# Kernel optimization log

Hardware: AMD Instinct MI355X
Metric: run time of the kernel (lower is better)

## Reference

```python
import jax, jax.numpy as jnp
import numpy as np

# e2m1 FP4 value table: sign bit in nibble MSB, values {0,0.5,1,1.5,2,3,4,6}
_E2M1 = jnp.array([0.0, 0.5, 1.0, 1.5, 2.0, 3.0, 4.0, 6.0,
                   -0.0, -0.5, -1.0, -1.5, -2.0, -3.0, -4.0, -6.0], dtype=jnp.float32)


def _dequant_fp4(packed, scales, group_size):
    """packed: [E, out, in//8] uint32; scales: [E, in//group_size, out] -> [E, out, in] f32."""
    shifts = jnp.arange(8, dtype=jnp.uint32) * 4  # nibble shift amounts 0,4,...,28
    nib = (packed[..., None] >> shifts) & jnp.uint32(0xF)  # [E, out, in//8, 8]
    E, O, P, _ = nib.shape
    nib = nib.reshape(E, O, P * 8).astype(jnp.int32)
    w = _E2M1[nib]  # [E, out, in] f32
    gids = jnp.arange(P * 8) // group_size  # group id per input column
    sc = jnp.transpose(scales, (0, 2, 1))[:, :, gids]  # [E, out, in]
    return w * sc


def setup_inputs() -> dict:
    E, H, I, T, K, G = 8, 2048, 1408, 2048, 2, 128
    key = jax.random.key(0)
    ks = jax.random.split(key, 9)
    x = jax.random.normal(ks[0], (T, H), dtype=jnp.float32)
    gate_packed = jax.random.bits(ks[1], (E, I, H // 8), dtype=jnp.uint32)
    up_packed = jax.random.bits(ks[2], (E, I, H // 8), dtype=jnp.uint32)
    down_packed = jax.random.bits(ks[3], (E, H, I // 8), dtype=jnp.uint32)
    gate_scales = jax.random.uniform(ks[4], (E, H // G, I), jnp.float32, 0.5, 1.5)
    up_scales = jax.random.uniform(ks[5], (E, H // G, I), jnp.float32, 0.5, 1.5)
    down_scales = jax.random.uniform(ks[6], (E, I // G, H), jnp.float32, 0.5, 1.5)
    topk_idx = jax.random.randint(ks[7], (T, K), 0, E, dtype=jnp.int32)
    w = jax.random.uniform(ks[8], (T, K), jnp.float32)
    topk_w = w / jnp.sum(w, axis=-1, keepdims=True)
    return {"x": x,
            "gate_packed": gate_packed, "gate_scales": gate_scales,
            "up_packed": up_packed, "up_scales": up_scales,
            "down_packed": down_packed, "down_scales": down_scales,
            "topk_idx": topk_idx, "topk_w": topk_w, "group_size": G}


def reference(x, gate_packed, gate_scales, up_packed, up_scales,
              down_packed, down_scales, topk_idx, topk_w, group_size):
    # Fused dequant (nibble unpack + e2m1 table + per-group scale) for all experts
    gate_w = _dequant_fp4(gate_packed, gate_scales, group_size)  # [E, I, H]
    up_w = _dequant_fp4(up_packed, up_scales, group_size)        # [E, I, H]
    down_w = _dequant_fp4(down_packed, down_scales, group_size)  # [E, H, I]
    # Grouped SwiGLU expert MLP (dense over E=8 experts, gather routed outputs)
    g = jnp.einsum('th,eih->eti', x, gate_w)
    u = jnp.einsum('th,eih->eti', x, up_w)
    h = jax.nn.silu(g) * u                                        # [E, T, I]
    y = jnp.einsum('eti,ehi->eth', h, down_w)                     # [E, T, H]
    T = x.shape[0]
    sel = y[topk_idx, jnp.arange(T)[:, None], :]                  # [T, K, H]
    return jnp.sum(sel * topk_w[..., None], axis=1)               # [T, H]
```

## Files before the change

kernel.cpp:

```cpp
#include <hip/hip_runtime.h>
#include <hip/hip_bf16.h>
#include <stdint.h>

#define E_ 8
#define H_ 2048
#define I_ 1408
#define T_ 2048
#define K_ 2
#define G_ 128

typedef __bf16 bf16;
typedef bf16 bf16x8 __attribute__((ext_vector_type(8)));
typedef float f32x4 __attribute__((ext_vector_type(4)));

__device__ __forceinline__ uint32_t prm(uint32_t hi, uint32_t lo, uint32_t sel) {
    return __builtin_amdgcn_perm(hi, lo, sel);
}

struct DequantTab { uint32_t thi0, thi1, tlo0, tlo1; };

__device__ __forceinline__ DequantTab build_tab(float s) {
    union { bf16 h[8]; uint32_t u[4]; } tb;
    tb.h[0] = (bf16)(0.0f);
    tb.h[1] = (bf16)(0.5f * s);
    tb.h[2] = (bf16)(1.0f * s);
    tb.h[3] = (bf16)(1.5f * s);
    tb.h[4] = (bf16)(2.0f * s);
    tb.h[5] = (bf16)(3.0f * s);
    tb.h[6] = (bf16)(4.0f * s);
    tb.h[7] = (bf16)(6.0f * s);
    DequantTab t;
    t.thi0 = prm(tb.u[1], tb.u[0], 0x07050301u);
    t.tlo0 = prm(tb.u[1], tb.u[0], 0x06040200u);
    t.thi1 = prm(tb.u[3], tb.u[2], 0x07050301u);
    t.tlo1 = prm(tb.u[3], tb.u[2], 0x06040200u);
    return t;
}

__device__ __forceinline__ uint4 dequant8t(uint32_t p, const DequantTab& t) {
    const uint32_t pr = p >> 4;
    const uint32_t pe = p  & 0x07070707u;
    const uint32_t po = pr & 0x07070707u;
    const uint32_t He = prm(t.thi1, t.thi0, pe) | ((p  & 0x08080808u) << 4);
    const uint32_t Le = prm(t.tlo1, t.tlo0, pe);
    const uint32_t Ho = prm(t.thi1, t.thi0, po) | ((pr & 0x08080808u) << 4);
    const uint32_t Lo = prm(t.tlo1, t.tlo0, po);
    const uint32_t E01 = prm(He, Le, 0x05010400u);
    const uint32_t E23 = prm(He, Le, 0x07030602u);
    const uint32_t O01 = prm(Ho, Lo, 0x05010400u);
    const uint32_t O23 = prm(Ho, Lo, 0x07030602u);
    return make_uint4(prm(O01, E01, 0x05040100u),
                      prm(O01, E01, 0x07060302u),
                      prm(O23, E23, 0x05040100u),
                      prm(O23, E23, 0x07060302u));
}

__device__ __forceinline__ void gld16(void* lds, const void* g) {
    __builtin_amdgcn_global_load_lds(
        (__attribute__((address_space(1))) void*)g,
        (__attribute__((address_space(3))) void*)lds, 16, 0, 0);
}

#define SB0() __builtin_amdgcn_sched_barrier(0)

#define DQW(WD, PW, TAB) do { \
    uint4 d0_ = dequant8t((PW).x, (TAB)); \
    uint4 d1_ = dequant8t((PW).y, (TAB)); \
    uint4 d2_ = dequant8t((PW).z, (TAB)); \
    uint4 d3_ = dequant8t((PW).w, (TAB)); \
    *(uint4*)&WD[wrow][((cb + 0) ^ rs) * 8] = d0_; \
    *(uint4*)&WD[wrow][((cb + 1) ^ rs) * 8] = d1_; \
    *(uint4*)&WD[wrow][((cb + 2) ^ rs) * 8] = d2_; \
    *(uint4*)&WD[wrow][((cb + 3) ^ rs) * 8] = d3_; \
} while (0)

__global__ void route_count(const int* __restrict__ topk_idx, int* __restrict__ counts) {
    int p = blockIdx.x * blockDim.x + threadIdx.x;
    if (p < T_ * K_) atomicAdd(&counts[topk_idx[p]], 1);
}

__global__ void route_scan(const int* __restrict__ counts, int* __restrict__ offsets,
                           int* __restrict__ tmap) {
    if (threadIdx.x == 0) {
        int acc = 0, ti = 0;
        for (int e = 0; e < E_; e++) {
            offsets[e] = acc;
            int nt = (counts[e] + 127) >> 7;
            for (int j = 0; j < nt; j++) tmap[ti++] = (e << 16) | j;
            acc += counts[e];
        }
        offsets[E_] = acc;
        offsets[E_ + 1] = ti;
        for (; ti < 64; ti++) tmap[ti] = -1;
    }
}

__global__ void route_fill(const int* __restrict__ topk_idx, const float* __restrict__ topk_w,
                           int* __restrict__ cursors, const int* __restrict__ offsets,
                           int* __restrict__ tok, float* __restrict__ wgt,
                           int* __restrict__ inv) {
    int p = blockIdx.x * blockDim.x + threadIdx.x;
    if (p < T_ * K_) {
        int e = topk_idx[p];
        int slot = atomicAdd(&cursors[e], 1);
        int idx = offsets[e] + slot;
        tok[idx] = p / K_;
        wgt[idx] = topk_w[p];
        inv[p] = idx;
    }
}

__global__ __launch_bounds__(256)
void xcast_kernel(const float* __restrict__ x, uint4* __restrict__ xb) {
    const int i = blockIdx.x * 256 + threadIdx.x;
    const float4 a = ((const float4*)x)[i * 2];
    const float4 b = ((const float4*)x)[i * 2 + 1];
    union { uint4 u; bf16 h[8]; } r;
    r.h[0] = (bf16)a.x; r.h[1] = (bf16)a.y; r.h[2] = (bf16)a.z; r.h[3] = (bf16)a.w;
    r.h[4] = (bf16)b.x; r.h[5] = (bf16)b.y; r.h[6] = (bf16)b.z; r.h[7] = (bf16)b.w;
    xb[i] = r.u;
}

__global__ __launch_bounds__(256, 2)
void gemm1t_kernel(const bf16* __restrict__ xb,
                   const uint32_t* __restrict__ gate_packed,
                   const float* __restrict__ gate_scales,
                   const uint32_t* __restrict__ up_packed,
                   const float* __restrict__ up_scales,
                   const int* __restrict__ offsets,
                   const int* __restrict__ tmap,
                   const int* __restrict__ tok, bf16* __restrict__ h_buf)
{
    __shared__ __align__(16) bf16 xs0[128][64];
    __shared__ __align__(16) bf16 xs1[128][64];
    __shared__ __align__(16) bf16 wgs0[64][64];
    __shared__ __align__(16) bf16 wgs1[64][64];
    __shared__ __align__(16) bf16 wus0[64][64];
    __shared__ __align__(16) bf16 wus1[64][64];

    const int tid = threadIdx.x;
    const int ntiles = offsets[E_ + 1];
    const int nwork = ntiles * 22;

    const int xr = tid >> 3;
    const int xc = tid & 7;
    const int xch = (xc ^ (xr & 7)) * 8;

    const int mat  = tid >> 7;
    const int id   = tid & 127;
    const int wrow = id >> 1;
    const int quad = id & 1;
    const int cb = quad * 4, rs = wrow & 7;

    const int wave = tid >> 6, lane = tid & 63;
    const int wy = wave >> 1, wx = wave & 1;
    const int lrow = lane & 15, kq = lane >> 4;

    constexpr int NG = H_ / G_;

#define MFMA1(XS, WG, WU) do { \
    _Pragma("unroll") \
    for (int kh = 0; kh < 2; ++kh) { \
        bf16x8 a[4], bg[2], bu[2]; \
        _Pragma("unroll") \
        for (int mi = 0; mi < 4; ++mi) { \
            const int ra = wy * 64 + mi * 16 + lrow; \
            a[mi] = *(const bf16x8*)&XS[ra][((kh * 4 + kq) ^ (ra & 7)) * 8]; \
        } \
        _Pragma("unroll") \
        for (int ni = 0; ni < 2; ++ni) { \
            const int rbq = wx * 32 + ni * 16 + lrow; \
            const int cbq = ((kh * 4 + kq) ^ (rbq & 7)) * 8; \
            bg[ni] = *(const bf16x8*)&WG[rbq][cbq]; \
            bu[ni] = *(const bf16x8*)&WU[rbq][cbq]; \
        } \
        _Pragma("unroll") \
        for (int mi = 0; mi < 4; ++mi) \
            _Pragma("unroll") \
            for (int ni = 0; ni < 2; ++ni) { \
                accg[mi][ni] = __builtin_amdgcn_mfma_f32_16x16x32_bf16(a[mi], bg[ni], accg[mi][ni], 0, 0, 0); \
                accu[mi][ni] = __builtin_amdgcn_mfma_f32_16x16x32_bf16(a[mi], bu[ni], accu[mi][ni], 0, 0, 0); \
            } \
    } \
} while (0)

    for (int wk = blockIdx.x; wk < nwork; wk += gridDim.x) {
        const int wt = wk / 22;
        const int itile = wk - wt * 22;
        const int tm = tmap[wt];
        const int e = tm >> 16, ty = tm & 0xffff;
        const int row0 = offsets[e];
        const int cnt = offsets[e + 1] - row0;

        const bf16* xsrc[4];
        bf16 *xdst0[4], *xdst1[4];
#pragma unroll
        for (int j = 0; j < 4; ++j) {
            int g = ty * 128 + xr + j * 32;
            g = (g < cnt) ? g : (cnt - 1);
            xsrc[j] = xb + (size_t)tok[row0 + g] * H_ + xch;
            xdst0[j] = &xs0[xr + j * 32][xc * 8];
            xdst1[j] = &xs1[xr + j * 32][xc * 8];
        }

        const int irow = itile * 64 + wrow;
        const uint32_t* wp_row = (mat ? up_packed : gate_packed)
            + (size_t)e * I_ * (H_ / 8) + (size_t)irow * (H_ / 8) + quad * 4;
        const float* ws_row = (mat ? up_scales : gate_scales)
            + (size_t)e * (H_ / G_) * I_ + irow;
        bf16 (* const wd0)[64] = mat ? wus0 : wgs0;
        bf16 (* const wd1)[64] = mat ? wus1 : wgs1;

        f32x4 accg[4][2] = {};
        f32x4 accu[4][2] = {};

#pragma unroll
        for (int j = 0; j < 4; ++j) gld16(xdst0[j], xsrc[j]);
        SB0();
        uint4 pw0 = *(const uint4*)(wp_row);
        uint4 pwO = *(const uint4*)(wp_row + 8);
        float sc0 = ws_row[0];
        SB0();
        DequantTab tab = build_tab(sc0);
        DQW(wd0, pw0, tab);
        asm volatile("s_waitcnt lgkmcnt(0)" ::: "memory");
        __builtin_amdgcn_s_barrier();
        SB0();

        float scn = 0.f;
        uint4 pwE;
        for (int kg = 0; kg < NG; ++kg) {
            const bool last = (kg == NG - 1);
#pragma unroll
            for (int j = 0; j < 4; ++j) gld16(xdst1[j], xsrc[j] + (kg * 2 + 1) * 64);
            SB0();
            if (!last) {
                pwE = *(const uint4*)(wp_row + (size_t)(kg * 2 + 2) * 8);
                scn = ws_row[(size_t)(kg + 1) * I_];
            }
            SB0();
            DQW(wd1, pwO, tab);
            MFMA1(xs0, wgs0, wus0);
            SB0();
            if (!last) asm volatile("s_waitcnt vmcnt(2) lgkmcnt(0)" ::: "memory");
            else       asm volatile("s_waitcnt vmcnt(0) lgkmcnt(0)" ::: "memory");
            __builtin_amdgcn_s_barrier();
            SB0();

            if (!last) {
#pragma unroll
                for (int j = 0; j < 4; ++j) gld16(xdst0[j], xsrc[j] + (kg * 2 + 2) * 64);
                SB0();
                pwO = *(const uint4*)(wp_row + (size_t)(kg * 2 + 3) * 8);
                SB0();
                tab = build_tab(scn);
                DQW(wd0, pwE, tab);
                MFMA1(xs1, wgs1, wus1);
                SB0();
                asm volatile("s_waitcnt vmcnt(1) lgkmcnt(0)" ::: "memory");
                __builtin_amdgcn_s_barrier();
                SB0();
            } else {
                MFMA1(xs1, wgs1, wus1);
                SB0();
                asm volatile("s_waitcnt lgkmcnt(0)" ::: "memory");
                __builtin_amdgcn_s_barrier();
                SB0();
            }
        }

#pragma unroll
        for (int mi = 0; mi < 4; ++mi)
#pragma unroll
            for (int ni = 0; ni < 2; ++ni) {
                const int icol = itile * 64 + wx * 32 + ni * 16 + lrow;
#pragma unroll
                for (int r = 0; r < 4; ++r) {
                    const int grow = ty * 128 + wy * 64 + mi * 16 + kq * 4 + r;
                    if (grow < cnt) {
                        const float gv = accg[mi][ni][r];
                        const float hv = gv / (1.f + __expf(-gv)) * accu[mi][ni][r];
                        h_buf[(size_t)(row0 + grow) * I_ + icol] = (bf16)hv;
                    }
                }
            }
        __builtin_amdgcn_s_barrier();
    }
#undef MFMA1
}

__global__ __launch_bounds__(256, 2)
void gemm2t_kernel(const bf16* __restrict__ h_buf,
                   const uint32_t* __restrict__ down_packed,
                   const float* __restrict__ down_scales,
                   const int* __restrict__ offsets,
                   const int* __restrict__ tmap,
                   const float* __restrict__ wgt, float* __restrict__ yp)
{
    __shared__ __align__(16) bf16 hs0[128][64];
    __shared__ __align__(16) bf16 hs1[128][64];
    __shared__ __align__(16) bf16 wds0[128][64];
    __shared__ __align__(16) bf16 wds1[128][64];

    const int tid = threadIdx.x;
    const int ntiles = offsets[E_ + 1];
    const int nwork = ntiles * 16;

    const int xr = tid >> 3;
    const int xc = tid & 7;
    const int xch = (xc ^ (xr & 7)) * 8;

    const int wrow = tid >> 1;
    const int quad = tid & 1;
    const int cb = quad * 4, rs = wrow & 7;

    const int wave = tid >> 6, lane = tid & 63;
    const int wy = wave >> 1, wx = wave & 1;
    const int lrow = lane & 15, kq = lane >> 4;

    constexpr int NG = I_ / G_;

#define MFMA2(HS, WD) do { \
    _Pragma("unroll") \
    for (int kh = 0; kh < 2; ++kh) { \
        bf16x8 a[4], b[4]; \
        _Pragma("unroll") \
        for (int mi = 0; mi < 4; ++mi) { \
            const int ra = wy * 64 + mi * 16 + lrow; \
            a[mi] = *(const bf16x8*)&HS[ra][((kh * 4 + kq) ^ (ra & 7)) * 8]; \
        } \
        _Pragma("unroll") \
        for (int ni = 0; ni < 4; ++ni) { \
            const int rbq = wx * 64 + ni * 16 + lrow; \
            b[ni] = *(const bf16x8*)&WD[rbq][((kh * 4 + kq) ^ (rbq & 7)) * 8]; \
        } \
        _Pragma("unroll") \
        for (int mi = 0; mi < 4; ++mi) \
            _Pragma("unroll") \
            for (int ni = 0; ni < 4; ++ni) \
                acc[mi][ni] = __builtin_amdgcn_mfma_f32_16x16x32_bf16(a[mi], b[ni], acc[mi][ni], 0, 0, 0); \
    } \
} while (0)

    for (int wk = blockIdx.x; wk < nwork; wk += gridDim.x) {
        const int wt = wk >> 4;
        const int htile = wk & 15;
        const int tm = tmap[wt];
        const int e = tm >> 16, ty = tm & 0xffff;
        const int row0 = offsets[e];
        const int cnt = offsets[e + 1] - row0;

        const bf16* hsrc[4];
        bf16 *hdst0[4], *hdst1[4];
#pragma unroll
        for (int j = 0; j < 4; ++j) {
            int g = ty * 128 + xr + j * 32;
            g = (g < cnt) ? g : (cnt - 1);
            hsrc[j] = h_buf + (size_t)(row0 + g) * I_ + xch;
            hdst0[j] = &hs0[xr + j * 32][xc * 8];
            hdst1[j] = &hs1[xr + j * 32][xc * 8];
        }

        const int hrow = htile * 128 + wrow;
        const uint32_t* dp_row = down_packed + (size_t)e * H_ * (I_ / 8) + (size_t)hrow * (I_ / 8) + quad * 4;
        const float* ds_row = down_scales + (size_t)e * (I_ / G_) * H_ + hrow;

        f32x4 acc[4][4] = {};

#pragma unroll
        for (int j = 0; j < 4; ++j) gld16(hdst0[j], hsrc[j]);
        SB0();
        uint4 pw0 = *(const uint4*)(dp_row);
        uint4 pwO = *(const uint4*)(dp_row + 8);
        float sc0 = ds_row[0];
        SB0();
        DequantTab tab = build_tab(sc0);
        DQW(wds0, pw0, tab);
        asm volatile("s_waitcnt lgkmcnt(0)" ::: "memory");
        __builtin_amdgcn_s_barrier();
        SB0();

        float scn = 0.f;
        uint4 pwE;
        for (int kg = 0; kg < NG; ++kg) {
            const bool last = (kg == NG - 1);
#pragma unroll
            for (int j = 0; j < 4; ++j) gld16(hdst1[j], hsrc[j] + (kg * 2 + 1) * 64);
            SB0();
            if (!last) {
                pwE = *(const uint4*)(dp_row + (size_t)(kg * 2 + 2) * 8);
                scn = ds_row[(size_t)(kg + 1) * H_];
            }
            SB0();
            DQW(wds1, pwO, tab);
            MFMA2(hs0, wds0);
            SB0();
            if (!last) asm volatile("s_waitcnt vmcnt(2) lgkmcnt(0)" ::: "memory");
            else       asm volatile("s_waitcnt vmcnt(0) lgkmcnt(0)" ::: "memory");
            __builtin_amdgcn_s_barrier();
            SB0();

            if (!last) {
#pragma unroll
                for (int j = 0; j < 4; ++j) gld16(hdst0[j], hsrc[j] + (kg * 2 + 2) * 64);
                SB0();
                pwO = *(const uint4*)(dp_row + (size_t)(kg * 2 + 3) * 8);
                SB0();
                tab = build_tab(scn);
                DQW(wds0, pwE, tab);
                MFMA2(hs1, wds1);
                SB0();
                asm volatile("s_waitcnt vmcnt(1) lgkmcnt(0)" ::: "memory");
                __builtin_amdgcn_s_barrier();
                SB0();
            } else {
                MFMA2(hs1, wds1);
                SB0();
                asm volatile("s_waitcnt lgkmcnt(0)" ::: "memory");
                __builtin_amdgcn_s_barrier();
                SB0();
            }
        }

#pragma unroll
        for (int mi = 0; mi < 4; ++mi)
#pragma unroll
            for (int r = 0; r < 4; ++r) {
                const int lr = wy * 64 + mi * 16 + kq * 4 + r;
                const int grow = ty * 128 + lr;
                if (grow < cnt) {
                    const float w = wgt[row0 + grow];
#pragma unroll
                    for (int ni = 0; ni < 4; ++ni) {
                        const int col = htile * 128 + wx * 64 + ni * 16 + lrow;
                        yp[(size_t)(row0 + grow) * H_ + col] = acc[mi][ni][r] * w;
                    }
                }
            }
        __builtin_amdgcn_s_barrier();
    }
#undef MFMA2
}

__global__ __launch_bounds__(256)
void combine_kernel(const float* __restrict__ yp, const int* __restrict__ inv,
                    float* __restrict__ out) {
    const int idx = blockIdx.x * 256 + threadIdx.x;
    const int t = idx >> 9;
    const int c = idx & 511;
    const float4 a = ((const float4*)yp)[(size_t)inv[t * 2] * (H_ / 4) + c];
    const float4 b = ((const float4*)yp)[(size_t)inv[t * 2 + 1] * (H_ / 4) + c];
    float4 o;
    o.x = a.x + b.x; o.y = a.y + b.y; o.z = a.z + b.z; o.w = a.w + b.w;
    ((float4*)out)[idx] = o;
}

extern "C" void kernel_launch(void* const* d_in, const int* in_sizes, int n_in,
                              void* d_out, int out_size, void* d_ws, size_t ws_size,
                              hipStream_t stream) {
    const float* x = (const float*)d_in[0];
    const uint32_t* gate_packed = (const uint32_t*)d_in[1];
    const float* gate_scales = (const float*)d_in[2];
    const uint32_t* up_packed = (const uint32_t*)d_in[3];
    const float* up_scales = (const float*)d_in[4];
    const uint32_t* down_packed = (const uint32_t*)d_in[5];
    const float* down_scales = (const float*)d_in[6];
    const int* topk_idx = (const int*)d_in[7];
    const float* topk_w = (const float*)d_in[8];
    float* out = (float*)d_out;

    char* ws = (char*)d_ws;
    int* counts  = (int*)ws;
    int* cursors = (int*)(ws + 32);
    int* offsets = (int*)(ws + 64);
    int* tmap    = (int*)(ws + 128);
    int* tok     = (int*)(ws + 640);
    float* wgt   = (float*)(ws + 17024);
    int* inv     = (int*)(ws + 33408);
    bf16* h_buf  = (bf16*)(ws + 49792);
    bf16* xb     = (bf16*)(ws + 49792 + 11534336ull);
    float* yp    = (float*)(ws + 49792 + 11534336ull + 8388608ull);

    hipMemsetAsync(d_ws, 0, 1024, stream);

    route_count<<<(T_ * K_ + 255) / 256, 256, 0, stream>>>(topk_idx, counts);
    route_scan<<<1, 64, 0, stream>>>(counts, offsets, tmap);
    route_fill<<<(T_ * K_ + 255) / 256, 256, 0, stream>>>(topk_idx, topk_w, cursors, offsets,
                                                          tok, wgt, inv);
    xcast_kernel<<<T_ * H_ / 8 / 256, 256, 0, stream>>>(x, (uint4*)xb);

    gemm1t_kernel<<<512, 256, 0, stream>>>(xb, gate_packed, gate_scales, up_packed, up_scales,
                                           offsets, tmap, tok, h_buf);
    gemm2t_kernel<<<512, 256, 0, stream>>>(h_buf, down_packed, down_scales,
                                           offsets, tmap, wgt, yp);
    combine_kernel<<<T_ * H_ / 4 / 256, 256, 0, stream>>>(yp, inv, out);
}
```

Before: 273.3 us.

## Fuse top-k combine into down GEMM via atomics; single-buffer weight tiles for occupancy

Result: slower. 286.1 us (+4.7%).

```diff
diff --git a/kernel.cpp b/kernel.cpp
--- a/kernel.cpp
+++ b/kernel.cpp
@@ -97,8 +97,7 @@
 
 __global__ void route_fill(const int* __restrict__ topk_idx, const float* __restrict__ topk_w,
                            int* __restrict__ cursors, const int* __restrict__ offsets,
-                           int* __restrict__ tok, float* __restrict__ wgt,
-                           int* __restrict__ inv) {
+                           int* __restrict__ tok, float* __restrict__ wgt) {
     int p = blockIdx.x * blockDim.x + threadIdx.x;
     if (p < T_ * K_) {
         int e = topk_idx[p];
@@ -106,7 +105,6 @@
         int idx = offsets[e] + slot;
         tok[idx] = p / K_;
         wgt[idx] = topk_w[p];
-        inv[p] = idx;
     }
 }
 
@@ -121,7 +119,7 @@
     xb[i] = r.u;
 }
 
-__global__ __launch_bounds__(256, 2)
+__global__ __launch_bounds__(256, 3)
 void gemm1t_kernel(const bf16* __restrict__ xb,
                    const uint32_t* __restrict__ gate_packed,
                    const float* __restrict__ gate_scales,
@@ -133,10 +131,8 @@
 {
     __shared__ __align__(16) bf16 xs0[128][64];
     __shared__ __align__(16) bf16 xs1[128][64];
-    __shared__ __align__(16) bf16 wgs0[64][64];
-    __shared__ __align__(16) bf16 wgs1[64][64];
-    __shared__ __align__(16) bf16 wus0[64][64];
-    __shared__ __align__(16) bf16 wus1[64][64];
+    __shared__ __align__(16) bf16 wgs[64][64];
+    __shared__ __align__(16) bf16 wus[64][64];
 
     const int tid = threadIdx.x;
     const int ntiles = offsets[E_ + 1];
@@ -157,8 +153,9 @@
     const int lrow = lane & 15, kq = lane >> 4;
 
     constexpr int NG = H_ / G_;
-
-#define MFMA1(XS, WG, WU) do { \
+    constexpr int NT = 2 * NG;
+
+#define MFMA1(XS) do { \
     _Pragma("unroll") \
     for (int kh = 0; kh < 2; ++kh) { \
         bf16x8 a[4], bg[2], bu[2]; \
@@ -171,8 +168,8 @@
         for (int ni = 0; ni < 2; ++ni) { \
             const int rbq = wx * 32 + ni * 16 + lrow; \
             const int cbq = ((kh * 4 + kq) ^ (rbq & 7)) * 8; \
-            bg[ni] = *(const bf16x8*)&WG[rbq][cbq]; \
-            bu[ni] = *(const bf16x8*)&WU[rbq][cbq]; \
+            bg[ni] = *(const bf16x8*)&wgs[rbq][cbq]; \
+            bu[ni] = *(const bf16x8*)&wus[rbq][cbq]; \
         } \
         _Pragma("unroll") \
         for (int mi = 0; mi < 4; ++mi) \
@@ -208,8 +205,7 @@
             + (size_t)e * I_ * (H_ / 8) + (size_t)irow * (H_ / 8) + quad * 4;
         const float* ws_row = (mat ? up_scales : gate_scales)
             + (size_t)e * (H_ / G_) * I_ + irow;
-        bf16 (* const wd0)[64] = mat ? wus0 : wgs0;
-        bf16 (* const wd1)[64] = mat ? wus1 : wgs1;
+        bf16 (* const wd)[64] = mat ? wus : wgs;
 
         f32x4 accg[4][2] = {};
         f32x4 accu[4][2] = {};
@@ -217,56 +213,44 @@
 #pragma unroll
         for (int j = 0; j < 4; ++j) gld16(xdst0[j], xsrc[j]);
         SB0();
-        uint4 pw0 = *(const uint4*)(wp_row);
-        uint4 pwO = *(const uint4*)(wp_row + 8);
-        float sc0 = ws_row[0];
+        uint4 pw = *(const uint4*)(wp_row);
+        float sc = ws_row[0];
         SB0();
-        DequantTab tab = build_tab(sc0);
-        DQW(wd0, pw0, tab);
-        asm volatile("s_waitcnt lgkmcnt(0)" ::: "memory");
-        __builtin_amdgcn_s_barrier();
-        SB0();
-
-        float scn = 0.f;
-        uint4 pwE;
+
+        float scn = sc;
+        uint4 pwn;
         for (int kg = 0; kg < NG; ++kg) {
-            const bool last = (kg == NG - 1);
-#pragma unroll
-            for (int j = 0; j < 4; ++j) gld16(xdst1[j], xsrc[j] + (kg * 2 + 1) * 64);
-            SB0();
-            if (!last) {
-                pwE = *(const uint4*)(wp_row + (size_t)(kg * 2 + 2) * 8);
-                scn = ws_row[(size_t)(kg + 1) * I_];
-            }
-            SB0();
-            DQW(wd1, pwO, tab);
-            MFMA1(xs0, wgs0, wus0);
-            SB0();
-            if (!last) asm volatile("s_waitcnt vmcnt(2) lgkmcnt(0)" ::: "memory");
-            else       asm volatile("s_waitcnt vmcnt(0) lgkmcnt(0)" ::: "memory");
-            __builtin_amdgcn_s_barrier();
-            SB0();
-
-            if (!last) {
-#pragma unroll
-                for (int j = 0; j < 4; ++j) gld16(xdst0[j], xsrc[j] + (kg * 2 + 2) * 64);
-                SB0();
-                pwO = *(const uint4*)(wp_row + (size_t)(kg * 2 + 3) * 8);
-                SB0();
-                tab = build_tab(scn);
-                DQW(wd0, pwE, tab);
-                MFMA1(xs1, wgs1, wus1);
-                SB0();
-                asm volatile("s_waitcnt vmcnt(1) lgkmcnt(0)" ::: "memory");
+            const DequantTab tab = build_tab(sc);
+#pragma unroll
+            for (int kh2 = 0; kh2 < 2; ++kh2) {
+                const int t = kg * 2 + kh2;
+                const bool lastT = (t == NT - 1);
+                if (!lastT) {
+                    bf16* const* xd = kh2 ? xdst0 : xdst1;
+#pragma unroll
+                    for (int j = 0; j < 4; ++j) gld16(xd[j], xsrc[j] + (t + 1) * 64);
+                    SB0();
+                    pwn = *(const uint4*)(wp_row + (size_t)(t + 1) * 8);
+                    if (kh2 == 0) {
+                        const int kgn = (kg + 1 < NG) ? kg + 1 : kg;
+                        scn = ws_row[(size_t)kgn * I_];
+                    }
+                    SB0();
+                }
+                DQW(wd, pw, tab);
+                SB0();
+                if (!lastT) asm volatile("s_waitcnt vmcnt(6) lgkmcnt(0)" ::: "memory");
+                else        asm volatile("s_waitcnt vmcnt(0) lgkmcnt(0)" ::: "memory");
                 __builtin_amdgcn_s_barrier();
                 SB0();
-            } else {
-                MFMA1(xs1, wgs1, wus1);
+                if (kh2 == 0) MFMA1(xs0); else MFMA1(xs1);
                 SB0();
                 asm volatile("s_waitcnt lgkmcnt(0)" ::: "memory");
                 __builtin_amdgcn_s_barrier();
                 SB0();
+                pw = pwn;
             }
+            sc = scn;
         }
 
 #pragma unroll
@@ -284,23 +268,22 @@
                     }
                 }
             }
-        __builtin_amdgcn_s_barrier();
     }
 #undef MFMA1
 }
 
-__global__ __launch_bounds__(256, 2)
+__global__ __launch_bounds__(256, 3)
 void gemm2t_kernel(const bf16* __restrict__ h_buf,
                    const uint32_t* __restrict__ down_packed,
                    const float* __restrict__ down_scales,
                    const int* __restrict__ offsets,
                    const int* __restrict__ tmap,
-                   const float* __restrict__ wgt, float* __restrict__ yp)
+                   const int* __restrict__ tok,
+                   const float* __restrict__ wgt, float* __restrict__ out)
 {
     __shared__ __align__(16) bf16 hs0[128][64];
     __shared__ __align__(16) bf16 hs1[128][64];
-    __shared__ __align__(16) bf16 wds0[128][64];
-    __shared__ __align__(16) bf16 wds1[128][64];
+    __shared__ __align__(16) bf16 wds[128][64];
 
     const int tid = threadIdx.x;
     const int ntiles = offsets[E_ + 1];
@@ -319,8 +302,9 @@
     const int lrow = lane & 15, kq = lane >> 4;
 
     constexpr int NG = I_ / G_;
-
-#define MFMA2(HS, WD) do { \
+    constexpr int NT = 2 * NG;
+
+#define MFMA2(HS) do { \
     _Pragma("unroll") \
     for (int kh = 0; kh < 2; ++kh) { \
         bf16x8 a[4], b[4]; \
@@ -332,7 +316,7 @@
         _Pragma("unroll") \
         for (int ni = 0; ni < 4; ++ni) { \
             const int rbq = wx * 64 + ni * 16 + lrow; \
-            b[ni] = *(const bf16x8*)&WD[rbq][((kh * 4 + kq) ^ (rbq & 7)) * 8]; \
+            b[ni] = *(const bf16x8*)&wds[rbq][((kh * 4 + kq) ^ (rbq & 7)) * 8]; \
         } \
         _Pragma("unroll") \
         for (int mi = 0; mi < 4; ++mi) \
@@ -370,89 +354,64 @@
 #pragma unroll
         for (int j = 0; j < 4; ++j) gld16(hdst0[j], hsrc[j]);
         SB0();
-        uint4 pw0 = *(const uint4*)(dp_row);
-        uint4 pwO = *(const uint4*)(dp_row + 8);
-        float sc0 = ds_row[0];
+        uint4 pw = *(const uint4*)(dp_row);
+        float sc = ds_row[0];
         SB0();
-        DequantTab tab = build_tab(sc0);
-        DQW(wds0, pw0, tab);
-        asm volatile("s_waitcnt lgkmcnt(0)" ::: "memory");
-        __builtin_amdgcn_s_barrier();
-        SB0();
-
-        float scn = 0.f;
-        uint4 pwE;
+
+        float scn = sc;
+        uint4 pwn;
         for (int kg = 0; kg < NG; ++kg) {
-            const bool last = (kg == NG - 1);
-#pragma unroll
-            for (int j = 0; j < 4; ++j) gld16(hdst1[j], hsrc[j] + (kg * 2 + 1) * 64);
-            SB0();
-            if (!last) {
-                pwE = *(const uint4*)(dp_row + (size_t)(kg * 2 + 2) * 8);
-                scn = ds_row[(size_t)(kg + 1) * H_];
-            }
-            SB0();
-            DQW(wds1, pwO, tab);
-            MFMA2(hs0, wds0);
-            SB0();
-            if (!last) asm volatile("s_waitcnt vmcnt(2) lgkmcnt(0)" ::: "memory");
-            else       asm volatile("s_waitcnt vmcnt(0) lgkmcnt(0)" ::: "memory");
-            __builtin_amdgcn_s_barrier();
-            SB0();
-
-            if (!last) {
-#pragma unroll
-                for (int j = 0; j < 4; ++j) gld16(hdst0[j], hsrc[j] + (kg * 2 + 2) * 64);
-                SB0();
-                pwO = *(const uint4*)(dp_row + (size_t)(kg * 2 + 3) * 8);
-                SB0();
-                tab = build_tab(scn);
-                DQW(wds0, pwE, tab);
-                MFMA2(hs1, wds1);
-                SB0();
-                asm volatile("s_waitcnt vmcnt(1) lgkmcnt(0)" ::: "memory");
+            const DequantTab tab = build_tab(sc);
+#pragma unroll
+            for (int kh2 = 0; kh2 < 2; ++kh2) {
+                const int t = kg * 2 + kh2;
+                const bool lastT = (t == NT - 1);
+                if (!lastT) {
+                    bf16* const* hd = kh2 ? hdst0 : hdst1;
+#pragma unroll
+                    for (int j = 0; j < 4; ++j) gld16(hd[j], hsrc[j] + (t + 1) * 64);
+                    SB0();
+                    pwn = *(const uint4*)(dp_row + (size_t)(t + 1) * 8);
+                    if (kh2 == 0) {
+                        const int kgn = (kg + 1 < NG) ? kg + 1 : kg;
+                        scn = ds_row[(size_t)kgn * H_];
+                    }
+                    SB0();
+                }
+                DQW(wds, pw, tab);
+                SB0();
+                if (!lastT) asm volatile("s_waitcnt vmcnt(6) lgkmcnt(0)" ::: "memory");
+                else        asm volatile("s_waitcnt vmcnt(0) lgkmcnt(0)" ::: "memory");
                 __builtin_amdgcn_s_barrier();
                 SB0();
-            } else {
-                MFMA2(hs1, wds1);
+                if (kh2 == 0) MFMA2(hs0); else MFMA2(hs1);
                 SB0();
                 asm volatile("s_waitcnt lgkmcnt(0)" ::: "memory");
                 __builtin_amdgcn_s_barrier();
                 SB0();
+                pw = pwn;
             }
+            sc = scn;
         }
 
 #pragma unroll
         for (int mi = 0; mi < 4; ++mi)
 #pragma unroll
             for (int r = 0; r < 4; ++r) {
-                const int lr = wy * 64 + mi * 16 + kq * 4 + r;
-                const int grow = ty * 128 + lr;
+                const int grow = ty * 128 + wy * 64 + mi * 16 + kq * 4 + r;
                 if (grow < cnt) {
-                    const float w = wgt[row0 + grow];
+                    const int slot = row0 + grow;
+                    const float w = wgt[slot];
+                    const int tk = tok[slot];
 #pragma unroll
                     for (int ni = 0; ni < 4; ++ni) {
                         const int col = htile * 128 + wx * 64 + ni * 16 + lrow;
-                        yp[(size_t)(row0 + grow) * H_ + col] = acc[mi][ni][r] * w;
+                        atomicAdd(out + (size_t)tk * H_ + col, acc[mi][ni][r] * w);
                     }
                 }
             }
-        __builtin_amdgcn_s_barrier();
     }
 #undef MFMA2
-}
-
-__global__ __launch_bounds__(256)
-void combine_kernel(const float* __restrict__ yp, const int* __restrict__ inv,
-                    float* __restrict__ out) {
-    const int idx = blockIdx.x * 256 + threadIdx.x;
-    const int t = idx >> 9;
-    const int c = idx & 511;
-    const float4 a = ((const float4*)yp)[(size_t)inv[t * 2] * (H_ / 4) + c];
-    const float4 b = ((const float4*)yp)[(size_t)inv[t * 2 + 1] * (H_ / 4) + c];
-    float4 o;
-    o.x = a.x + b.x; o.y = a.y + b.y; o.z = a.z + b.z; o.w = a.w + b.w;
-    ((float4*)out)[idx] = o;
 }
 
 extern "C" void kernel_launch(void* const* d_in, const int* in_sizes, int n_in,
@@ -476,22 +435,20 @@
     int* tmap    = (int*)(ws + 128);
     int* tok     = (int*)(ws + 640);
     float* wgt   = (float*)(ws + 17024);
-    int* inv     = (int*)(ws + 33408);
     bf16* h_buf  = (bf16*)(ws + 49792);
     bf16* xb     = (bf16*)(ws + 49792 + 11534336ull);
-    float* yp    = (float*)(ws + 49792 + 11534336ull + 8388608ull);
 
     hipMemsetAsync(d_ws, 0, 1024, stream);
+    hipMemsetAsync(d_out, 0, out_size, stream);
 
     route_count<<<(T_ * K_ + 255) / 256, 256, 0, stream>>>(topk_idx, counts);
     route_scan<<<1, 64, 0, stream>>>(counts, offsets, tmap);
     route_fill<<<(T_ * K_ + 255) / 256, 256, 0, stream>>>(topk_idx, topk_w, cursors, offsets,
-                                                          tok, wgt, inv);
+                                                          tok, wgt);
     xcast_kernel<<<T_ * H_ / 8 / 256, 256, 0, stream>>>(x, (uint4*)xb);
 
-    gemm1t_kernel<<<512, 256, 0, stream>>>(xb, gate_packed, gate_scales, up_packed, up_scales,
+    gemm1t_kernel<<<768, 256, 0, stream>>>(xb, gate_packed, gate_scales, up_packed, up_scales,
                                            offsets, tmap, tok, h_buf);
-    gemm2t_kernel<<<512, 256, 0, stream>>>(h_buf, down_packed, down_scales,
-                                           offsets, tmap, wgt, yp);
-    combine_kernel<<<T_ * H_ / 4 / 256, 256, 0, stream>>>(yp, inv, out);
-}
+    gemm2t_kernel<<<768, 256, 0, stream>>>(h_buf, down_packed, down_scales,
+                                           offsets, tmap, tok, wgt, out);
+}
```
